# Optimization experiments

Measured on AMD Instinct MI355X. Metric: run time of the kernel, lower is better.

The kernel has to match this reference:

```python
import jax, jax.numpy as jnp
import numpy as np

B, T, D = 4, 50, 512
SRC, SENTS, WORDS = 400, 16, 40
NEG = jnp.float32(-1e30)  # stands in for -inf mask fill (numerically identical post-softmax)


def _seq_mask(lengths, max_len):
    # [n, max_len] bool, True where position < length
    return jnp.arange(max_len)[None, :] < lengths[:, None]


def _mlp_score(q, h, Wq, bq, Uc, v):
    # Bahdanau additive score: v^T tanh(W q + U h)
    # q: [b,t,d], h: [b,s,d] -> [b,t,s]
    wq = q @ Wq + bq                       # [b,t,d]
    uh = h @ Uc                            # [b,s,d]
    wquh = jnp.tanh(wq[:, :, None, :] + uh[:, None, :, :])  # [b,t,s,d]
    return jnp.einsum('btsd,d->bts', wquh, v)


def setup_inputs() -> dict:
    key = jax.random.key(0)
    ks = jax.random.split(key, 20)
    s = np.float32(1.0 / np.sqrt(D))
    def p(k, shape):
        return jax.random.normal(k, shape, jnp.float32) * s
    return {
        'source': jax.random.normal(ks[0], (B, T, D), jnp.float32),
        'src_bank': jax.random.normal(ks[1], (SRC, B, D), jnp.float32),
        'src_lengths': jax.random.randint(ks[2], (B,), 1, SRC + 1),
        'qa_sent_bank': jax.random.normal(ks[3], (SENTS, B, D), jnp.float32),
        'qa_sent_lengths': jax.random.randint(ks[4], (B,), 1, SENTS + 1),
        'qa_word_bank': jax.random.normal(ks[5], (WORDS, B, SENTS, D), jnp.float32),
        'qa_word_lengths': jax.random.randint(ks[6], (B, SENTS), 1, WORDS + 1),
        'Wq_word': p(ks[7], (D, D)), 'bq_word': jnp.zeros((D,), jnp.float32),
        'Uc_word': p(ks[8], (D, D)), 'v_word': p(ks[9], (D,)),
        'Wq_sent': p(ks[10], (D, D)), 'bq_sent': jnp.zeros((D,), jnp.float32),
        'Uc_sent': p(ks[11], (D, D)), 'v_sent': p(ks[12], (D,)),
        'Wq_pass': p(ks[13], (D, D)), 'bq_pass': jnp.zeros((D,), jnp.float32),
        'Uc_pass': p(ks[14], (D, D)), 'v_pass': p(ks[15], (D,)),
    }


def _forward(source, src_bank, qa_sent_bank, qa_word_bank,
             Wq_word, bq_word, Uc_word, v_word,
             Wq_sent, bq_sent, Uc_sent, v_sent,
             Wq_pass, bq_pass, Uc_pass, v_pass,
             src_lengths, qa_word_lengths):
    b = source.shape[0]
    # [words,b,sents,d] -> [b,sents,words,d] -> [b, sents*words, d]
    qa_word = jnp.transpose(qa_word_bank, (1, 2, 0, 3)).reshape(b, SENTS * WORDS, D)
    src = jnp.transpose(src_bank, (1, 0, 2))       # [b,src,d]
    sent = jnp.transpose(qa_sent_bank, (1, 0, 2))  # [b,sents,d]

    qa_word_align = _mlp_score(source, qa_word, Wq_word, bq_word, Uc_word, v_word)  # [b,t,sents*words]
    src_align = _mlp_score(source, src, Wq_pass, bq_pass, Uc_pass, v_pass)          # [b,t,src]
    qa_sent_align = _mlp_score(source, sent, Wq_sent, bq_sent, Uc_sent, v_sent)     # [b,t,sents]

    # hierarchical combination: word score scaled by its sentence score
    qa_hier = (qa_word_align.reshape(b, T, SENTS, WORDS)
               * qa_sent_align[..., None]).reshape(b, T, SENTS * WORDS)

    align = jnp.concatenate([src_align, qa_hier], axis=-1)  # [b,t,src+sents*words]

    qa_mask = _seq_mask(qa_word_lengths.reshape(-1), WORDS).reshape(b, SENTS * WORDS)[:, None, :]
    src_mask = _seq_mask(src_lengths, SRC)[:, None, :]
    mask = jnp.concatenate([src_mask, qa_mask], axis=-1)

    align = jnp.where(mask, align, NEG)
    align_vectors = jax.nn.softmax(align, axis=-1)  # joint length-masked softmax

    memory = jnp.concatenate([src, qa_word], axis=1)          # [b, src+sents*words, d]
    c = jnp.einsum('bts,bsd->btd', align_vectors, memory)     # weighted context sum
    return c


def reference(source, src_bank, src_lengths, qa_sent_bank, qa_sent_lengths,
              qa_word_bank, qa_word_lengths,
              Wq_word, bq_word, Uc_word, v_word,
              Wq_sent, bq_sent, Uc_sent, v_sent,
              Wq_pass, bq_pass, Uc_pass, v_pass):
    # qa_sent_lengths is accepted but unused, matching the original forward()
    return _forward(source, src_bank, qa_sent_bank, qa_word_bank,
                    Wq_word, bq_word, Uc_word, v_word,
                    Wq_sent, bq_sent, Uc_sent, v_sent,
                    Wq_pass, bq_pass, Uc_pass, v_pass,
                    src_lengths, qa_word_lengths)
```

## Files before the change

### kernel.cpp

```cpp
#include <hip/hip_runtime.h>
#include <hip/hip_bf16.h>


#define B_    4
#define T_    50
#define D_    512
#define SRC_  400
#define SENTS_ 16
#define WORDS_ 40
#define NW_   640
#define NMEM_ 1040
#define NK_   1056
#define NJOB_ 1056

#define C2L2E 2.8853900817779268f

typedef unsigned short ushort_t;
using s8v = __attribute__((ext_vector_type(8))) short;
using f4v = __attribute__((ext_vector_type(4))) float;

#define OFF_WQ_WORD 0
#define OFF_WQ_SENT 102400
#define OFF_WQ_PASS 204800
#define OFF_UH_SRC  307200
#define OFF_UH_WORD 1126400
#define OFF_UH_SENT 2437120
#define OFF_SC_SRC  2469888
#define OFF_SC_WORD 2549888
#define OFF_SC_SENT 2677888
#define P_BYTE_OFF  10724352ull
#define MT_BYTE_OFF 11265024ull
#define WT_BYTE_OFF 15590400ull

__device__ __forceinline__ ushort_t f2b(float f) {
    __hip_bfloat16 h = __float2bfloat16(f);
    return *(ushort_t*)&h;
}

__global__ __launch_bounds__(256) void k0f_transpose(
    const float* __restrict__ w0, const float* __restrict__ w1,
    const float* __restrict__ w2, const float* __restrict__ w3,
    const float* __restrict__ w4, const float* __restrict__ w5,
    const float* __restrict__ src_bank, const float* __restrict__ qa_word_bank,
    ushort_t* __restrict__ wt, ushort_t* __restrict__ mt)
{
    __shared__ float tile[32][33];
    int z = blockIdx.z;
    int tx = threadIdx.x & 31, ty = threadIdx.x >> 5;
    if (z < 6) {
        if (blockIdx.x >= 16) return;
        const float* W;
        switch (z) {
            case 0: W = w0; break; case 1: W = w1; break; case 2: W = w2; break;
            case 3: W = w3; break; case 4: W = w4; break; default: W = w5; break;
        }
        ushort_t* Wt = wt + z * (D_ * D_);
        int n0 = blockIdx.x * 32, k0 = blockIdx.y * 32;
#pragma unroll
        for (int a = 0; a < 4; ++a)
            tile[ty + a * 8][tx] = W[(k0 + ty + a * 8) * D_ + n0 + tx];
        __syncthreads();
#pragma unroll
        for (int a = 0; a < 4; ++a)
            Wt[(n0 + ty + a * 8) * D_ + k0 + tx] = f2b(tile[tx][ty + a * 8]);
    } else {
        int b = z - 6;
        int s0 = blockIdx.x * 32, d0 = blockIdx.y * 32;
#pragma unroll
        for (int a = 0; a < 4; ++a) {
            int s = s0 + ty + a * 8;
            float val = 0.f;
            if (s < SRC_) {
                val = src_bank[(s * B_ + b) * D_ + d0 + tx];
            } else if (s < NMEM_) {
                int j = s - SRC_; int se = j / WORDS_; int wd = j - se * WORDS_;
                val = qa_word_bank[((wd * B_ + b) * SENTS_ + se) * D_ + d0 + tx];
            }
            tile[ty + a * 8][tx] = val;
        }
        __syncthreads();
        ushort_t* base = mt + (size_t)b * D_ * NK_;
#pragma unroll
        for (int a = 0; a < 4; ++a) {
            int d = d0 + ty + a * 8;
            base[(size_t)d * NK_ + s0 + tx] = f2b(tile[tx][ty + a * 8]);
        }
    }
}

__global__ __launch_bounds__(256) void k1_gemm(
    const float* __restrict__ source, const float* __restrict__ src_bank,
    const float* __restrict__ qa_sent_bank, const float* __restrict__ qa_word_bank,
    const ushort_t* __restrict__ wt,
    const float* __restrict__ bq_word, const float* __restrict__ bq_sent,
    const float* __restrict__ bq_pass,
    float* __restrict__ wsf)
{
    __shared__ short At[64 * 32];
    __shared__ short Bt[64 * 32];
    int z = blockIdx.z;
    int M, atype; const float* bias; float* C;
    switch (z) {
        case 0: M = 200;  atype = 0; bias = bq_word; C = wsf + OFF_WQ_WORD; break;
        case 1: M = 200;  atype = 0; bias = bq_sent; C = wsf + OFF_WQ_SENT; break;
        case 2: M = 200;  atype = 0; bias = bq_pass; C = wsf + OFF_WQ_PASS; break;
        case 3: M = 2560; atype = 1; bias = nullptr; C = wsf + OFF_UH_WORD; break;
        case 4: M = 1600; atype = 2; bias = nullptr; C = wsf + OFF_UH_SRC;  break;
        default: M = 64;  atype = 3; bias = nullptr; C = wsf + OFF_UH_SENT; break;
    }
    int m0 = blockIdx.y * 64;
    if (m0 >= M) return;
    int n0 = blockIdx.x * 64;
    const ushort_t* W = wt + z * (D_ * D_);

    int tid = threadIdx.x;
    int lane = tid & 63, wv = tid >> 6;
    int quad = lane >> 4, l16 = lane & 15;
    int sm = tid >> 2, koff = (tid & 3) * 8;

    const float* arow = nullptr;
    {
        int r = m0 + sm;
        if (r < M) {
            if (atype == 0) arow = source + r * D_;
            else if (atype == 1) { int b = r / NW_; int j = r - b * NW_;
                                   int se = j / WORDS_; int wd = j - se * WORDS_;
                                   arow = qa_word_bank + ((wd * B_ + b) * SENTS_ + se) * D_; }
            else if (atype == 2) { int b = r / SRC_; int j = r - b * SRC_;
                                   arow = src_bank + (j * B_ + b) * D_; }
            else                 { int b = r >> 4; int s2 = r & 15;
                                   arow = qa_sent_bank + (s2 * B_ + b) * D_; }
        }
    }
    const ushort_t* wrow = W + (n0 + sm) * D_;

    f4v acc[4] = { {0.f,0.f,0.f,0.f}, {0.f,0.f,0.f,0.f},
                   {0.f,0.f,0.f,0.f}, {0.f,0.f,0.f,0.f} };

    for (int kk = 0; kk < 16; ++kk) {
        int k0 = kk * 32;
        union { ushort_t u[8]; int4 v; } pk;
        if (arow) {
            float4 f0 = *(const float4*)(arow + k0 + koff);
            float4 f1 = *(const float4*)(arow + k0 + koff + 4);
            pk.u[0] = f2b(f0.x); pk.u[1] = f2b(f0.y);
            pk.u[2] = f2b(f0.z); pk.u[3] = f2b(f0.w);
            pk.u[4] = f2b(f1.x); pk.u[5] = f2b(f1.y);
            pk.u[6] = f2b(f1.z); pk.u[7] = f2b(f1.w);
        } else {
            pk.v = int4{0, 0, 0, 0};
        }
        int4 bv = *(const int4*)(wrow + k0 + koff);
        *(int4*)(At + sm * 32 + koff) = pk.v;
        *(int4*)(Bt + sm * 32 + koff) = bv;
        __syncthreads();
        s8v af = *(const s8v*)(At + (wv * 16 + l16) * 32 + quad * 8);
#pragma unroll
        for (int ng = 0; ng < 4; ++ng) {
            s8v bf = *(const s8v*)(Bt + (ng * 16 + l16) * 32 + quad * 8);
            acc[ng] = __builtin_amdgcn_mfma_f32_16x16x32_bf16(af, bf, acc[ng], 0, 0, 0);
        }
        __syncthreads();
    }
#pragma unroll
    for (int ng = 0; ng < 4; ++ng) {
        int col = n0 + ng * 16 + l16;
        float bb = bias ? bias[col] : 0.f;
#pragma unroll
        for (int rr = 0; rr < 4; ++rr) {
            int row = m0 + wv * 16 + quad * 4 + rr;
            if (row < M) C[row * D_ + col] = (acc[ng][rr] + bb) * C2L2E;
        }
    }
}

__global__ __launch_bounds__(256) void k2_scores(
    const float* __restrict__ v_word, const float* __restrict__ v_sent,
    const float* __restrict__ v_pass,
    const int* __restrict__ src_lengths, const int* __restrict__ qa_word_lengths,
    float* __restrict__ wsf)
{
    int lane = threadIdx.x & 63;
    int job2 = blockIdx.x * 4 + (threadIdx.x >> 6);
    int job = job2 >> 1, th = job2 & 1;
    int b = job / NJOB_, slot = job - b * NJOB_;
    const float* uh; const float* v; const float* wq; float* out; int ostride;
    if (slot < SRC_) {
        if (slot >= src_lengths[b]) return;
        uh = wsf + OFF_UH_SRC + (b * SRC_ + slot) * D_;
        v = v_pass; wq = wsf + OFF_WQ_PASS + b * T_ * D_;
        out = wsf + OFF_SC_SRC + b * T_ * SRC_ + slot; ostride = SRC_;
    } else if (slot < NMEM_) {
        int j = slot - SRC_;
        int se = j / WORDS_; int wd = j - se * WORDS_;
        if (wd >= qa_word_lengths[b * SENTS_ + se]) return;
        uh = wsf + OFF_UH_WORD + (b * NW_ + j) * D_;
        v = v_word; wq = wsf + OFF_WQ_WORD + b * T_ * D_;
        out = wsf + OFF_SC_WORD + b * T_ * NW_ + j; ostride = NW_;
    } else {
        int s2 = slot - NMEM_;
        uh = wsf + OFF_UH_SENT + (b * SENTS_ + s2) * D_;
        v = v_sent; wq = wsf + OFF_WQ_SENT + b * T_ * D_;
        out = wsf + OFF_SC_SENT + b * T_ * SENTS_ + s2; ostride = SENTS_;
    }
    int d0 = lane * 8;
    float4 u0 = *(const float4*)(uh + d0);
    float4 u1 = *(const float4*)(uh + d0 + 4);
    float uhr[8] = {u0.x, u0.y, u0.z, u0.w, u1.x, u1.y, u1.z, u1.w};
    float4 v0 = *(const float4*)(v + d0);
    float4 v1 = *(const float4*)(v + d0 + 4);
    float vr[8] = {v0.x, v0.y, v0.z, v0.w, v1.x, v1.y, v1.z, v1.w};

    float vs = ((vr[0] + vr[1]) + (vr[2] + vr[3])) + ((vr[4] + vr[5]) + (vr[6] + vr[7]));
#pragma unroll
    for (int off = 32; off > 0; off >>= 1) vs += __shfl_xor(vs, off, 64);

    const float* wqh = wq + th * 25 * D_;
    float acc[25];
#pragma unroll 1
    for (int c = 0; c < 5; ++c) {
#pragma unroll
        for (int u5 = 0; u5 < 5; ++u5) {
            int u = c * 5 + u5;
            const float* wr = wqh + u * D_ + d0;
            float4 w0 = *(const float4*)(wr);
            float4 w1 = *(const float4*)(wr + 4);
            float wrr[8] = {w0.x, w0.y, w0.z, w0.w, w1.x, w1.y, w1.z, w1.w};
            float a = 0.f;
#pragma unroll
            for (int j = 0; j < 8; ++j) {
                float e = __builtin_amdgcn_exp2f(wrr[j] + uhr[j]);
                float r = __builtin_amdgcn_rcpf(e + 1.f);
                a = fmaf(vr[j], r, a);
            }
            acc[u] = a;
        }
    }
#pragma unroll
    for (int off = 32; off > 0; off >>= 1) {
#pragma unroll
        for (int u = 0; u < 25; ++u)
            acc[u] += __shfl_xor(acc[u], off, 64);
    }
    if (lane == 0) {
#pragma unroll
        for (int u = 0; u < 25; ++u)
            out[(th * 25 + u) * ostride] = fmaf(-2.f, acc[u], vs);
    }
}

__global__ __launch_bounds__(256) void k3a_softmax(
    const int* __restrict__ src_lengths, const int* __restrict__ qa_word_lengths,
    const float* __restrict__ wsf, ushort_t* __restrict__ P)
{
    __shared__ float p[NMEM_];
    __shared__ float red[4];
    int tid = threadIdx.x, lane = tid & 63, wv = tid >> 6;
    int bt = blockIdx.x, b = bt / T_, t = bt - b * T_;
    const float* sc_src  = wsf + OFF_SC_SRC  + bt * SRC_;
    const float* sc_word = wsf + OFF_SC_WORD + bt * NW_;
    const float* sc_sent = wsf + OFF_SC_SENT + bt * SENTS_;
    int slen = src_lengths[b];
    float mx = -3.0e38f;
    for (int j = tid; j < NMEM_; j += 256) {
        float val;
        if (j < SRC_) {
            val = (j < slen) ? sc_src[j] : -1e30f;
        } else {
            int jj = j - SRC_; int se = jj / WORDS_; int wd = jj - se * WORDS_;
            float raw = sc_word[jj] * sc_sent[se];
            val = (wd < qa_word_lengths[b * SENTS_ + se]) ? raw : -1e30f;
        }
        p[j] = val;
        mx = fmaxf(mx, val);
    }
#pragma unroll
    for (int off = 32; off > 0; off >>= 1) mx = fmaxf(mx, __shfl_xor(mx, off, 64));
    if (lane == 0) red[wv] = mx;
    __syncthreads();
    mx = fmaxf(fmaxf(red[0], red[1]), fmaxf(red[2], red[3]));
    __syncthreads();
    float lsum = 0.f;
    for (int j = tid; j < NMEM_; j += 256) {
        float e = __expf(p[j] - mx);
        p[j] = e; lsum += e;
    }
#pragma unroll
    for (int off = 32; off > 0; off >>= 1) lsum += __shfl_xor(lsum, off, 64);
    if (lane == 0) red[wv] = lsum;
    __syncthreads();
    float inv = 1.f / (red[0] + red[1] + red[2] + red[3]);
    ushort_t* prow = P + (size_t)(b * 64 + t) * NK_;
    for (int j = tid; j < NK_; j += 256)
        prow[j] = (j < NMEM_) ? f2b(p[j] * inv) : (ushort_t)0;
}

__global__ __launch_bounds__(256) void k3c_gemm(
    const ushort_t* __restrict__ P, const ushort_t* __restrict__ Mt,
    float* __restrict__ out)
{
    __shared__ short At[64 * 32];
    __shared__ short Bt[32 * 32];
    int b = blockIdx.y;
    int n0 = blockIdx.x * 32;
    int tid = threadIdx.x;
    int lane = tid & 63, wv = tid >> 6;
    int quad = lane >> 4, l16 = lane & 15;
    int smA = tid >> 2, koffA = (tid & 3) * 8;
    int smB = tid >> 3, koffB = (tid & 7) * 4;

    const ushort_t* arow = P + (size_t)(b * 64 + smA) * NK_ + koffA;
    const ushort_t* brow = Mt + ((size_t)(b * D_ + n0 + smB)) * NK_ + koffB;

    f4v acc[2] = { {0.f,0.f,0.f,0.f}, {0.f,0.f,0.f,0.f} };

    for (int kk = 0; kk < 33; ++kk) {
        int k0 = kk * 32;
        int4 av = *(const int4*)(arow + k0);
        int2 bv = *(const int2*)(brow + k0);
        *(int4*)(At + smA * 32 + koffA) = av;
        *(int2*)(Bt + smB * 32 + koffB) = bv;
        __syncthreads();
        s8v af = *(const s8v*)(At + (wv * 16 + l16) * 32 + quad * 8);
#pragma unroll
        for (int ng = 0; ng < 2; ++ng) {
            s8v bf = *(const s8v*)(Bt + (ng * 16 + l16) * 32 + quad * 8);
            acc[ng] = __builtin_amdgcn_mfma_f32_16x16x32_bf16(af, bf, acc[ng], 0, 0, 0);
        }
        __syncthreads();
    }
#pragma unroll
    for (int ng = 0; ng < 2; ++ng) {
        int col = n0 + ng * 16 + l16;
#pragma unroll
        for (int rr = 0; rr < 4; ++rr) {
            int row = wv * 16 + quad * 4 + rr;
            if (row < T_) out[(size_t)(b * T_ + row) * D_ + col] = acc[ng][rr];
        }
    }
}

extern "C" void kernel_launch(void* const* d_in, const int* in_sizes, int n_in,
                              void* d_out, int out_size, void* d_ws, size_t ws_size,
                              hipStream_t stream)
{
    (void)in_sizes; (void)n_in; (void)out_size; (void)ws_size;
    const float* source          = (const float*)d_in[0];
    const float* src_bank        = (const float*)d_in[1];
    const int*   src_lengths     = (const int*)d_in[2];
    const float* qa_sent_bank    = (const float*)d_in[3];
    const float* qa_word_bank    = (const float*)d_in[5];
    const int*   qa_word_lengths = (const int*)d_in[6];
    const float* Wq_word = (const float*)d_in[7];
    const float* bq_word = (const float*)d_in[8];
    const float* Uc_word = (const float*)d_in[9];
    const float* v_word  = (const float*)d_in[10];
    const float* Wq_sent = (const float*)d_in[11];
    const float* bq_sent = (const float*)d_in[12];
    const float* Uc_sent = (const float*)d_in[13];
    const float* v_sent  = (const float*)d_in[14];
    const float* Wq_pass = (const float*)d_in[15];
    const float* bq_pass = (const float*)d_in[16];
    const float* Uc_pass = (const float*)d_in[17];
    const float* v_pass  = (const float*)d_in[18];

    float* wsf = (float*)d_ws;
    ushort_t* Pb  = (ushort_t*)((char*)d_ws + P_BYTE_OFF);
    ushort_t* mt  = (ushort_t*)((char*)d_ws + MT_BYTE_OFF);
    ushort_t* wt  = (ushort_t*)((char*)d_ws + WT_BYTE_OFF);
    float* out = (float*)d_out;

    k0f_transpose<<<dim3(33, 16, 10), dim3(256), 0, stream>>>(
        Wq_word, Wq_sent, Wq_pass, Uc_word, Uc_pass, Uc_sent,
        src_bank, qa_word_bank, wt, mt);
    k1_gemm<<<dim3(8, 40, 6), dim3(256), 0, stream>>>(
        source, src_bank, qa_sent_bank, qa_word_bank, wt,
        bq_word, bq_sent, bq_pass, wsf);
    k2_scores<<<dim3(NJOB_ * 2), dim3(256), 0, stream>>>(
        v_word, v_sent, v_pass, src_lengths, qa_word_lengths, wsf);
    k3a_softmax<<<dim3(200), dim3(256), 0, stream>>>(src_lengths, qa_word_lengths, wsf, Pb);
    k3c_gemm<<<dim3(16, 4), dim3(256), 0, stream>>>(Pb, mt, out);
}
```

Baseline: 166.1 us.

## Fuse weight transpose into projection GEMM and softmax into context GEMM

The separate weight-transpose kernel is removed: the projection GEMM now reads fp32 weights directly, stages them through a swizzled shared tile, converts them to bf16 in the B-operand layout, and software-pipelines global loads one to two k-steps ahead. The memory-transpose blocks are folded into the same launch. The softmax kernel and its bf16 probability buffer are removed: the context GEMM computes per-row max and sum itself, then builds the exp-normalised probabilities on the fly while double-buffering score and memory loads. The score kernel now reduces in groups of five to cut register pressure. This saves two launches and the P and Wt round trips, but the 64 context blocks each recompute softmax statistics and do exp work inside the GEMM loop.

```diff
diff --git a/kernel.cpp b/kernel.cpp
--- a/kernel.cpp
+++ b/kernel.cpp
@@ -28,44 +28,33 @@
 #define OFF_SC_SRC  2469888
 #define OFF_SC_WORD 2549888
 #define OFF_SC_SENT 2677888
-#define P_BYTE_OFF  10724352ull
 #define MT_BYTE_OFF 11265024ull
-#define WT_BYTE_OFF 15590400ull
 
 __device__ __forceinline__ ushort_t f2b(float f) {
     __hip_bfloat16 h = __float2bfloat16(f);
     return *(ushort_t*)&h;
 }
 
-__global__ __launch_bounds__(256) void k0f_transpose(
+__global__ __launch_bounds__(256) void kA(
+    const float* __restrict__ source, const float* __restrict__ src_bank,
+    const float* __restrict__ qa_sent_bank, const float* __restrict__ qa_word_bank,
     const float* __restrict__ w0, const float* __restrict__ w1,
     const float* __restrict__ w2, const float* __restrict__ w3,
     const float* __restrict__ w4, const float* __restrict__ w5,
-    const float* __restrict__ src_bank, const float* __restrict__ qa_word_bank,
-    ushort_t* __restrict__ wt, ushort_t* __restrict__ mt)
+    const float* __restrict__ bq_word, const float* __restrict__ bq_sent,
+    const float* __restrict__ bq_pass,
+    float* __restrict__ wsf, ushort_t* __restrict__ mt)
 {
-    __shared__ float tile[32][33];
-    int z = blockIdx.z;
-    int tx = threadIdx.x & 31, ty = threadIdx.x >> 5;
-    if (z < 6) {
-        if (blockIdx.x >= 16) return;
-        const float* W;
-        switch (z) {
-            case 0: W = w0; break; case 1: W = w1; break; case 2: W = w2; break;
-            case 3: W = w3; break; case 4: W = w4; break; default: W = w5; break;
-        }
-        ushort_t* Wt = wt + z * (D_ * D_);
-        int n0 = blockIdx.x * 32, k0 = blockIdx.y * 32;
-#pragma unroll
-        for (int a = 0; a < 4; ++a)
-            tile[ty + a * 8][tx] = W[(k0 + ty + a * 8) * D_ + n0 + tx];
-        __syncthreads();
-#pragma unroll
-        for (int a = 0; a < 4; ++a)
-            Wt[(n0 + ty + a * 8) * D_ + k0 + tx] = f2b(tile[tx][ty + a * 8]);
-    } else {
-        int b = z - 6;
-        int s0 = blockIdx.x * 32, d0 = blockIdx.y * 32;
+    __shared__ float smemf[4224];
+    int bid = blockIdx.x;
+    int tid = threadIdx.x;
+
+    if (bid >= 1920) {
+        int tb = bid - 1920;
+        int b = tb / 528, r = tb - b * 528;
+        int s0 = (r % 33) * 32, d0 = (r / 33) * 32;
+        float (*tile)[33] = (float(*)[33])smemf;
+        int tx = tid & 31, ty = tid >> 5;
 #pragma unroll
         for (int a = 0; a < 4; ++a) {
             int s = s0 + ty + a * 8;
@@ -85,76 +74,113 @@
             int d = d0 + ty + a * 8;
             base[(size_t)d * NK_ + s0 + tx] = f2b(tile[tx][ty + a * 8]);
         }
-    }
-}
-
-__global__ __launch_bounds__(256) void k1_gemm(
-    const float* __restrict__ source, const float* __restrict__ src_bank,
-    const float* __restrict__ qa_sent_bank, const float* __restrict__ qa_word_bank,
-    const ushort_t* __restrict__ wt,
-    const float* __restrict__ bq_word, const float* __restrict__ bq_sent,
-    const float* __restrict__ bq_pass,
-    float* __restrict__ wsf)
-{
-    __shared__ short At[64 * 32];
-    __shared__ short Bt[64 * 32];
-    int z = blockIdx.z;
-    int M, atype; const float* bias; float* C;
+        return;
+    }
+
+    int z = bid / 320, rem = bid - z * 320;
+    int by = rem >> 3, bx = rem & 7;
+    int M, atype; const float* bias; const float* W; float* C;
     switch (z) {
-        case 0: M = 200;  atype = 0; bias = bq_word; C = wsf + OFF_WQ_WORD; break;
-        case 1: M = 200;  atype = 0; bias = bq_sent; C = wsf + OFF_WQ_SENT; break;
-        case 2: M = 200;  atype = 0; bias = bq_pass; C = wsf + OFF_WQ_PASS; break;
-        case 3: M = 2560; atype = 1; bias = nullptr; C = wsf + OFF_UH_WORD; break;
-        case 4: M = 1600; atype = 2; bias = nullptr; C = wsf + OFF_UH_SRC;  break;
-        default: M = 64;  atype = 3; bias = nullptr; C = wsf + OFF_UH_SENT; break;
-    }
-    int m0 = blockIdx.y * 64;
+        case 0: M = 200;  atype = 0; bias = bq_word; W = w0; C = wsf + OFF_WQ_WORD; break;
+        case 1: M = 200;  atype = 0; bias = bq_sent; W = w1; C = wsf + OFF_WQ_SENT; break;
+        case 2: M = 200;  atype = 0; bias = bq_pass; W = w2; C = wsf + OFF_WQ_PASS; break;
+        case 3: M = 2560; atype = 1; bias = nullptr; W = w3; C = wsf + OFF_UH_WORD; break;
+        case 4: M = 1600; atype = 2; bias = nullptr; W = w4; C = wsf + OFF_UH_SRC;  break;
+        default: M = 64;  atype = 3; bias = nullptr; W = w5; C = wsf + OFF_UH_SENT; break;
+    }
+    int m0 = by * 64;
     if (m0 >= M) return;
-    int n0 = blockIdx.x * 64;
-    const ushort_t* W = wt + z * (D_ * D_);
-
-    int tid = threadIdx.x;
-    int lane = tid & 63, wv = tid >> 6;
-    int quad = lane >> 4, l16 = lane & 15;
+    int n0 = bx * 64;
+
+    int lane = tid & 63, wvx = tid >> 6, quad = lane >> 4, l16 = lane & 15;
     int sm = tid >> 2, koff = (tid & 3) * 8;
+    int rW = tid >> 3, cW = (tid & 7) * 8;
+    int rWs = rW * 68 + (cW ^ (((rW >> 3) & 3) << 4));
+    int nB = tid >> 2, kB8 = (tid & 3) * 8;
+    int colp = nB ^ (((kB8 >> 3) & 3) << 4);
+
+    short* At = (short*)smemf;
+    short* Bt = (short*)(smemf + 1024);
+    float* Wtmp = smemf + 2048;
 
     const float* arow = nullptr;
     {
-        int r = m0 + sm;
-        if (r < M) {
-            if (atype == 0) arow = source + r * D_;
-            else if (atype == 1) { int b = r / NW_; int j = r - b * NW_;
+        int rr = m0 + sm;
+        if (rr < M) {
+            if (atype == 0) arow = source + rr * D_;
+            else if (atype == 1) { int b = rr / NW_; int j = rr - b * NW_;
                                    int se = j / WORDS_; int wd = j - se * WORDS_;
                                    arow = qa_word_bank + ((wd * B_ + b) * SENTS_ + se) * D_; }
-            else if (atype == 2) { int b = r / SRC_; int j = r - b * SRC_;
+            else if (atype == 2) { int b = rr / SRC_; int j = rr - b * SRC_;
                                    arow = src_bank + (j * B_ + b) * D_; }
-            else                 { int b = r >> 4; int s2 = r & 15;
+            else                 { int b = rr >> 4; int s2 = rr & 15;
                                    arow = qa_sent_bank + (s2 * B_ + b) * D_; }
         }
     }
-    const ushort_t* wrow = W + (n0 + sm) * D_;
+    const float* wbase = W + n0 + cW;
+
+    auto loadA = [&](float* r, int kk) {
+        if (arow) {
+            float4 f0 = *(const float4*)(arow + kk * 32 + koff);
+            float4 f1 = *(const float4*)(arow + kk * 32 + koff + 4);
+            r[0]=f0.x; r[1]=f0.y; r[2]=f0.z; r[3]=f0.w;
+            r[4]=f1.x; r[5]=f1.y; r[6]=f1.z; r[7]=f1.w;
+        } else {
+#pragma unroll
+            for (int i = 0; i < 8; ++i) r[i] = 0.f;
+        }
+    };
+    auto loadW = [&](float* r, int kk) {
+        const float* p = wbase + (kk * 32 + rW) * D_;
+        float4 f0 = *(const float4*)p;
+        float4 f1 = *(const float4*)(p + 4);
+        r[0]=f0.x; r[1]=f0.y; r[2]=f0.z; r[3]=f0.w;
+        r[4]=f1.x; r[5]=f1.y; r[6]=f1.z; r[7]=f1.w;
+    };
+    auto storeWtmp = [&](const float* r) {
+        *(float4*)(Wtmp + rWs)     = float4{r[0], r[1], r[2], r[3]};
+        *(float4*)(Wtmp + rWs + 4) = float4{r[4], r[5], r[6], r[7]};
+    };
+    auto storeAt = [&](const float* r) {
+        union { ushort_t u[8]; int4 v; } pk;
+#pragma unroll
+        for (int i = 0; i < 8; ++i) pk.u[i] = f2b(r[i]);
+        *(int4*)(At + sm * 32 + koff) = pk.v;
+    };
+    auto buildBt = [&]() {
+        union { ushort_t u[8]; int4 v; } pk;
+#pragma unroll
+        for (int i = 0; i < 8; ++i) pk.u[i] = f2b(Wtmp[(kB8 + i) * 68 + colp]);
+        *(int4*)(Bt + nB * 32 + kB8) = pk.v;
+    };
 
     f4v acc[4] = { {0.f,0.f,0.f,0.f}, {0.f,0.f,0.f,0.f},
                    {0.f,0.f,0.f,0.f}, {0.f,0.f,0.f,0.f} };
 
+    float ac[8], an[8], wn[8];
+    loadA(ac, 0);
+    {
+        float w0r[8];
+        loadW(w0r, 0);
+        storeWtmp(w0r);
+    }
+    loadW(wn, 1);
+    loadA(an, 1);
+    __syncthreads();
+
+#pragma unroll
     for (int kk = 0; kk < 16; ++kk) {
-        int k0 = kk * 32;
-        union { ushort_t u[8]; int4 v; } pk;
-        if (arow) {
-            float4 f0 = *(const float4*)(arow + k0 + koff);
-            float4 f1 = *(const float4*)(arow + k0 + koff + 4);
-            pk.u[0] = f2b(f0.x); pk.u[1] = f2b(f0.y);
-            pk.u[2] = f2b(f0.z); pk.u[3] = f2b(f0.w);
-            pk.u[4] = f2b(f1.x); pk.u[5] = f2b(f1.y);
-            pk.u[6] = f2b(f1.z); pk.u[7] = f2b(f1.w);
-        } else {
-            pk.v = int4{0, 0, 0, 0};
-        }
-        int4 bv = *(const int4*)(wrow + k0 + koff);
-        *(int4*)(At + sm * 32 + koff) = pk.v;
-        *(int4*)(Bt + sm * 32 + koff) = bv;
+        storeAt(ac);
+        buildBt();
         __syncthreads();
-        s8v af = *(const s8v*)(At + (wv * 16 + l16) * 32 + quad * 8);
+        if (kk < 15) storeWtmp(wn);
+        if (kk < 14) loadW(wn, kk + 2);
+        if (kk < 15) {
+#pragma unroll
+            for (int i = 0; i < 8; ++i) ac[i] = an[i];
+        }
+        if (kk < 14) loadA(an, kk + 2);
+        s8v af = *(const s8v*)(At + (wvx * 16 + l16) * 32 + quad * 8);
 #pragma unroll
         for (int ng = 0; ng < 4; ++ng) {
             s8v bf = *(const s8v*)(Bt + (ng * 16 + l16) * 32 + quad * 8);
@@ -162,19 +188,20 @@
         }
         __syncthreads();
     }
+
 #pragma unroll
     for (int ng = 0; ng < 4; ++ng) {
         int col = n0 + ng * 16 + l16;
         float bb = bias ? bias[col] : 0.f;
 #pragma unroll
-        for (int rr = 0; rr < 4; ++rr) {
-            int row = m0 + wv * 16 + quad * 4 + rr;
-            if (row < M) C[row * D_ + col] = (acc[ng][rr] + bb) * C2L2E;
+        for (int rr2 = 0; rr2 < 4; ++rr2) {
+            int row = m0 + wvx * 16 + quad * 4 + rr2;
+            if (row < M) C[row * D_ + col] = (acc[ng][rr2] + bb) * C2L2E;
         }
     }
 }
 
-__global__ __launch_bounds__(256) void k2_scores(
+__global__ __launch_bounds__(256) void kB_scores(
     const float* __restrict__ v_word, const float* __restrict__ v_sent,
     const float* __restrict__ v_pass,
     const int* __restrict__ src_lengths, const int* __restrict__ qa_word_lengths,
@@ -216,13 +243,12 @@
     for (int off = 32; off > 0; off >>= 1) vs += __shfl_xor(vs, off, 64);
 
     const float* wqh = wq + th * 25 * D_;
-    float acc[25];
 #pragma unroll 1
-    for (int c = 0; c < 5; ++c) {
+    for (int g = 0; g < 5; ++g) {
+        float a5[5];
 #pragma unroll
         for (int u5 = 0; u5 < 5; ++u5) {
-            int u = c * 5 + u5;
-            const float* wr = wqh + u * D_ + d0;
+            const float* wr = wqh + (g * 5 + u5) * D_ + d0;
             float4 w0 = *(const float4*)(wr);
             float4 w1 = *(const float4*)(wr + 4);
             float wrr[8] = {w0.x, w0.y, w0.z, w0.w, w1.x, w1.y, w1.z, w1.w};
@@ -233,109 +259,163 @@
                 float r = __builtin_amdgcn_rcpf(e + 1.f);
                 a = fmaf(vr[j], r, a);
             }
-            acc[u] = a;
-        }
-    }
-#pragma unroll
-    for (int off = 32; off > 0; off >>= 1) {
-#pragma unroll
-        for (int u = 0; u < 25; ++u)
-            acc[u] += __shfl_xor(acc[u], off, 64);
-    }
-    if (lane == 0) {
-#pragma unroll
-        for (int u = 0; u < 25; ++u)
-            out[(th * 25 + u) * ostride] = fmaf(-2.f, acc[u], vs);
+            a5[u5] = a;
+        }
+#pragma unroll
+        for (int off = 32; off > 0; off >>= 1) {
+#pragma unroll
+            for (int u5 = 0; u5 < 5; ++u5) a5[u5] += __shfl_xor(a5[u5], off, 64);
+        }
+        if (lane == 0) {
+#pragma unroll
+            for (int u5 = 0; u5 < 5; ++u5)
+                out[(th * 25 + g * 5 + u5) * ostride] = fmaf(-2.f, a5[u5], vs);
+        }
     }
 }
 
-__global__ __launch_bounds__(256) void k3a_softmax(
+__global__ __launch_bounds__(256) void kC_ctx(
     const int* __restrict__ src_lengths, const int* __restrict__ qa_word_lengths,
-    const float* __restrict__ wsf, ushort_t* __restrict__ P)
-{
-    __shared__ float p[NMEM_];
-    __shared__ float red[4];
-    int tid = threadIdx.x, lane = tid & 63, wv = tid >> 6;
-    int bt = blockIdx.x, b = bt / T_, t = bt - b * T_;
-    const float* sc_src  = wsf + OFF_SC_SRC  + bt * SRC_;
-    const float* sc_word = wsf + OFF_SC_WORD + bt * NW_;
-    const float* sc_sent = wsf + OFF_SC_SENT + bt * SENTS_;
-    int slen = src_lengths[b];
-    float mx = -3.0e38f;
-    for (int j = tid; j < NMEM_; j += 256) {
-        float val;
-        if (j < SRC_) {
-            val = (j < slen) ? sc_src[j] : -1e30f;
-        } else {
-            int jj = j - SRC_; int se = jj / WORDS_; int wd = jj - se * WORDS_;
-            float raw = sc_word[jj] * sc_sent[se];
-            val = (wd < qa_word_lengths[b * SENTS_ + se]) ? raw : -1e30f;
-        }
-        p[j] = val;
-        mx = fmaxf(mx, val);
-    }
-#pragma unroll
-    for (int off = 32; off > 0; off >>= 1) mx = fmaxf(mx, __shfl_xor(mx, off, 64));
-    if (lane == 0) red[wv] = mx;
-    __syncthreads();
-    mx = fmaxf(fmaxf(red[0], red[1]), fmaxf(red[2], red[3]));
-    __syncthreads();
-    float lsum = 0.f;
-    for (int j = tid; j < NMEM_; j += 256) {
-        float e = __expf(p[j] - mx);
-        p[j] = e; lsum += e;
-    }
-#pragma unroll
-    for (int off = 32; off > 0; off >>= 1) lsum += __shfl_xor(lsum, off, 64);
-    if (lane == 0) red[wv] = lsum;
-    __syncthreads();
-    float inv = 1.f / (red[0] + red[1] + red[2] + red[3]);
-    ushort_t* prow = P + (size_t)(b * 64 + t) * NK_;
-    for (int j = tid; j < NK_; j += 256)
-        prow[j] = (j < NMEM_) ? f2b(p[j] * inv) : (ushort_t)0;
-}
-
-__global__ __launch_bounds__(256) void k3c_gemm(
-    const ushort_t* __restrict__ P, const ushort_t* __restrict__ Mt,
+    const float* __restrict__ wsf, const ushort_t* __restrict__ Mt,
     float* __restrict__ out)
 {
     __shared__ short At[64 * 32];
     __shared__ short Bt[32 * 32];
-    int b = blockIdx.y;
-    int n0 = blockIdx.x * 32;
-    int tid = threadIdx.x;
-    int lane = tid & 63, wv = tid >> 6;
+    __shared__ float sentsL[T_ * SENTS_];
+    __shared__ float mxL[64];
+    __shared__ float invL[64];
+    __shared__ int lensL[SENTS_];
+    int tid = threadIdx.x, lane = tid & 63, wvx = tid >> 6;
     int quad = lane >> 4, l16 = lane & 15;
+    int b = blockIdx.y, n0 = blockIdx.x * 32;
+    int slen = src_lengths[b];
+
+    for (int i = tid; i < T_ * SENTS_; i += 256)
+        sentsL[i] = wsf[OFF_SC_SENT + b * (T_ * SENTS_) + i];
+    if (tid < SENTS_) lensL[tid] = qa_word_lengths[b * SENTS_ + tid];
+    if (tid >= 50 && tid < 64) { mxL[tid] = 0.f; invL[tid] = 0.f; }
+    __syncthreads();
+
+    const float* scs_b = wsf + OFF_SC_SRC + b * (T_ * SRC_);
+    const float* scw_b = wsf + OFF_SC_WORD + b * (T_ * NW_);
+
+    for (int t0 = wvx; t0 < T_; t0 += 8) {
+#pragma unroll
+        for (int tt = 0; tt < 2; ++tt) {
+            int t = t0 + tt * 4;
+            if (t < T_) {
+                const float* scs = scs_b + t * SRC_;
+                const float* scw = scw_b + t * NW_;
+                const float* srow = sentsL + t * SENTS_;
+                float vals[17];
+                float mxl = -3.0e38f;
+#pragma unroll
+                for (int i = 0; i < 17; ++i) {
+                    int j = lane + i * 64;
+                    float val = -1e30f;
+                    if (j < SRC_) {
+                        if (j < slen) val = scs[j];
+                    } else if (j < NMEM_) {
+                        int jj = j - SRC_; int se = jj / WORDS_; int wd = jj - se * WORDS_;
+                        if (wd < lensL[se]) val = scw[jj] * srow[se];
+                    }
+                    vals[i] = val;
+                    mxl = fmaxf(mxl, val);
+                }
+#pragma unroll
+                for (int off = 32; off > 0; off >>= 1)
+                    mxl = fmaxf(mxl, __shfl_xor(mxl, off, 64));
+                float s = 0.f;
+#pragma unroll
+                for (int i = 0; i < 17; ++i) s += __expf(vals[i] - mxl);
+#pragma unroll
+                for (int off = 32; off > 0; off >>= 1) s += __shfl_xor(s, off, 64);
+                if (lane == 0) { mxL[t] = mxl; invL[t] = 1.f / s; }
+            }
+        }
+    }
+    __syncthreads();
+
     int smA = tid >> 2, koffA = (tid & 3) * 8;
     int smB = tid >> 3, koffB = (tid & 7) * 4;
-
-    const ushort_t* arow = P + (size_t)(b * 64 + smA) * NK_ + koffA;
+    bool rowOK = smA < T_;
+    float mxT = mxL[smA], invT = invL[smA];
+    const float* scs = scs_b + (rowOK ? smA : 0) * SRC_;
+    const float* scw = scw_b + (rowOK ? smA : 0) * NW_;
+    const float* srowA = sentsL + (rowOK ? smA : 0) * SENTS_;
     const ushort_t* brow = Mt + ((size_t)(b * D_ + n0 + smB)) * NK_ + koffB;
 
-    f4v acc[2] = { {0.f,0.f,0.f,0.f}, {0.f,0.f,0.f,0.f} };
+    auto loadS = [&](float* r, int kk) {
+        int j0 = kk * 32 + koffA;
+        if (rowOK && j0 < NMEM_) {
+            const float* p = (j0 < SRC_) ? (scs + j0) : (scw + (j0 - SRC_));
+            float4 f0 = *(const float4*)p;
+            float4 f1 = *(const float4*)(p + 4);
+            r[0]=f0.x; r[1]=f0.y; r[2]=f0.z; r[3]=f0.w;
+            r[4]=f1.x; r[5]=f1.y; r[6]=f1.z; r[7]=f1.w;
+        } else {
+#pragma unroll
+            for (int i = 0; i < 8; ++i) r[i] = 0.f;
+        }
+    };
+    auto buildAt = [&](const float* r, int kk) {
+        int j0 = kk * 32 + koffA;
+        union { ushort_t u[8]; int4 v; } pk;
+        if (rowOK && j0 < NMEM_) {
+            if (j0 < SRC_) {
+#pragma unroll
+                for (int e = 0; e < 8; ++e) {
+                    float p = (j0 + e < slen) ? __expf(r[e] - mxT) * invT : 0.f;
+                    pk.u[e] = f2b(p);
+                }
+            } else {
+                int jj0 = j0 - SRC_;
+#pragma unroll
+                for (int e = 0; e < 8; ++e) {
+                    int jj = jj0 + e; int se = jj / WORDS_; int wd = jj - se * WORDS_;
+                    float p = (wd < lensL[se]) ? __expf(r[e] * srowA[se] - mxT) * invT : 0.f;
+                    pk.u[e] = f2b(p);
+                }
+            }
+        } else {
+            pk.v = int4{0, 0, 0, 0};
+        }
+        *(int4*)(At + smA * 32 + koffA) = pk.v;
+    };
+
+    f4v acc2[2] = { {0.f,0.f,0.f,0.f}, {0.f,0.f,0.f,0.f} };
+    float sc[8], sn[8];
+    int2 bc, bn;
+    loadS(sc, 0);
+    bc = *(const int2*)(brow);
 
     for (int kk = 0; kk < 33; ++kk) {
-        int k0 = kk * 32;
-        int4 av = *(const int4*)(arow + k0);
-        int2 bv = *(const int2*)(brow + k0);
-        *(int4*)(At + smA * 32 + koffA) = av;
-        *(int2*)(Bt + smB * 32 + koffB) = bv;
+        buildAt(sc, kk);
+        *(int2*)(Bt + smB * 32 + koffB) = bc;
         __syncthreads();
-        s8v af = *(const s8v*)(At + (wv * 16 + l16) * 32 + quad * 8);
+        if (kk < 32) {
+            loadS(sn, kk + 1);
+            bn = *(const int2*)(brow + (kk + 1) * 32);
+        }
+        s8v af = *(const s8v*)(At + (wvx * 16 + l16) * 32 + quad * 8);
 #pragma unroll
         for (int ng = 0; ng < 2; ++ng) {
             s8v bf = *(const s8v*)(Bt + (ng * 16 + l16) * 32 + quad * 8);
-            acc[ng] = __builtin_amdgcn_mfma_f32_16x16x32_bf16(af, bf, acc[ng], 0, 0, 0);
+            acc2[ng] = __builtin_amdgcn_mfma_f32_16x16x32_bf16(af, bf, acc2[ng], 0, 0, 0);
         }
         __syncthreads();
-    }
+#pragma unroll
+        for (int i = 0; i < 8; ++i) sc[i] = sn[i];
+        bc = bn;
+    }
+
 #pragma unroll
     for (int ng = 0; ng < 2; ++ng) {
         int col = n0 + ng * 16 + l16;
 #pragma unroll
-        for (int rr = 0; rr < 4; ++rr) {
-            int row = wv * 16 + quad * 4 + rr;
-            if (row < T_) out[(size_t)(b * T_ + row) * D_ + col] = acc[ng][rr];
+        for (int rr2 = 0; rr2 < 4; ++rr2) {
+            int row = wvx * 16 + quad * 4 + rr2;
+            if (row < T_) out[(size_t)(b * T_ + row) * D_ + col] = acc2[ng][rr2];
         }
     }
 }
@@ -365,19 +445,15 @@
     const float* v_pass  = (const float*)d_in[18];
 
     float* wsf = (float*)d_ws;
-    ushort_t* Pb  = (ushort_t*)((char*)d_ws + P_BYTE_OFF);
-    ushort_t* mt  = (ushort_t*)((char*)d_ws + MT_BYTE_OFF);
-    ushort_t* wt  = (ushort_t*)((char*)d_ws + WT_BYTE_OFF);
+    ushort_t* mt = (ushort_t*)((char*)d_ws + MT_BYTE_OFF);
     float* out = (float*)d_out;
 
-    k0f_transpose<<<dim3(33, 16, 10), dim3(256), 0, stream>>>(
+    kA<<<dim3(4032), dim3(256), 0, stream>>>(
+        source, src_bank, qa_sent_bank, qa_word_bank,
         Wq_word, Wq_sent, Wq_pass, Uc_word, Uc_pass, Uc_sent,
-        src_bank, qa_word_bank, wt, mt);
-    k1_gemm<<<dim3(8, 40, 6), dim3(256), 0, stream>>>(
-        source, src_bank, qa_sent_bank, qa_word_bank, wt,
-        bq_word, bq_sent, bq_pass, wsf);
-    k2_scores<<<dim3(NJOB_ * 2), dim3(256), 0, stream>>>(
+        bq_word, bq_sent, bq_pass, wsf, mt);
+    kB_scores<<<dim3(NJOB_ * 2), dim3(256), 0, stream>>>(
         v_word, v_sent, v_pass, src_lengths, qa_word_lengths, wsf);
-    k3a_softmax<<<dim3(200), dim3(256), 0, stream>>>(src_lengths, qa_word_lengths, wsf, Pb);
-    k3c_gemm<<<dim3(16, 4), dim3(256), 0, stream>>>(Pb, mt, out);
+    kC_ctx<<<dim3(16, 4), dim3(256), 0, stream>>>(
+        src_lengths, qa_word_lengths, wsf, mt, out);
 }
```

Result: slower. 218.1 us (+31.3%).

## Compact launch grids, prefetch GEMM tiles in registers, and chunk score reductions

Applied to the files above, without the earlier changes.

Replaces the 3D launch grids of the transpose and projection GEMM kernels with flat 1D grids that map block ids to work directly, so idle early-exit blocks are no longer launched. Adds register prefetching of global tiles two or three k-steps ahead in both bf16 MFMA GEMM loops, so global loads overlap the MFMA work instead of sitting just before the barrier. The score kernel now reduces and stores in groups of five rows rather than holding 25 accumulators, which lowers register pressure. The cost is more live registers for the prefetch buffers and extra index arithmetic.

```diff
diff --git a/kernel.cpp b/kernel.cpp
--- a/kernel.cpp
+++ b/kernel.cpp
@@ -45,17 +45,17 @@
     ushort_t* __restrict__ wt, ushort_t* __restrict__ mt)
 {
     __shared__ float tile[32][33];
-    int z = blockIdx.z;
+    int bid = blockIdx.x;
     int tx = threadIdx.x & 31, ty = threadIdx.x >> 5;
-    if (z < 6) {
-        if (blockIdx.x >= 16) return;
+    if (bid < 1536) {
+        int z = bid >> 8, r = bid & 255;
+        int n0 = (r & 15) * 32, k0 = (r >> 4) * 32;
         const float* W;
         switch (z) {
             case 0: W = w0; break; case 1: W = w1; break; case 2: W = w2; break;
             case 3: W = w3; break; case 4: W = w4; break; default: W = w5; break;
         }
         ushort_t* Wt = wt + z * (D_ * D_);
-        int n0 = blockIdx.x * 32, k0 = blockIdx.y * 32;
 #pragma unroll
         for (int a = 0; a < 4; ++a)
             tile[ty + a * 8][tx] = W[(k0 + ty + a * 8) * D_ + n0 + tx];
@@ -64,8 +64,9 @@
         for (int a = 0; a < 4; ++a)
             Wt[(n0 + ty + a * 8) * D_ + k0 + tx] = f2b(tile[tx][ty + a * 8]);
     } else {
-        int b = z - 6;
-        int s0 = blockIdx.x * 32, d0 = blockIdx.y * 32;
+        int tb = bid - 1536;
+        int b = tb / 528, r = tb - b * 528;
+        int s0 = (r % 33) * 32, d0 = (r / 33) * 32;
 #pragma unroll
         for (int a = 0; a < 4; ++a) {
             int s = s0 + ty + a * 8;
@@ -98,7 +99,13 @@
 {
     __shared__ short At[64 * 32];
     __shared__ short Bt[64 * 32];
-    int z = blockIdx.z;
+    int bid = blockIdx.x;
+    int z, rem;
+    if (bid < 96)       { z = bid >> 5; rem = bid & 31; }
+    else if (bid < 416) { z = 3; rem = bid - 96; }
+    else if (bid < 616) { z = 4; rem = bid - 416; }
+    else                { z = 5; rem = bid - 616; }
+    int by = rem >> 3, bx = rem & 7;
     int M, atype; const float* bias; float* C;
     switch (z) {
         case 0: M = 200;  atype = 0; bias = bq_word; C = wsf + OFF_WQ_WORD; break;
@@ -108,9 +115,7 @@
         case 4: M = 1600; atype = 2; bias = nullptr; C = wsf + OFF_UH_SRC;  break;
         default: M = 64;  atype = 3; bias = nullptr; C = wsf + OFF_UH_SENT; break;
     }
-    int m0 = blockIdx.y * 64;
-    if (m0 >= M) return;
-    int n0 = blockIdx.x * 64;
+    int m0 = by * 64, n0 = bx * 64;
     const ushort_t* W = wt + z * (D_ * D_);
 
     int tid = threadIdx.x;
@@ -134,26 +139,40 @@
     }
     const ushort_t* wrow = W + (n0 + sm) * D_;
 
+    auto loadA = [&](float* r, int kk) {
+        if (arow) {
+            float4 f0 = *(const float4*)(arow + kk * 32 + koff);
+            float4 f1 = *(const float4*)(arow + kk * 32 + koff + 4);
+            r[0]=f0.x; r[1]=f0.y; r[2]=f0.z; r[3]=f0.w;
+            r[4]=f1.x; r[5]=f1.y; r[6]=f1.z; r[7]=f1.w;
+        } else {
+#pragma unroll
+            for (int i = 0; i < 8; ++i) r[i] = 0.f;
+        }
+    };
+
     f4v acc[4] = { {0.f,0.f,0.f,0.f}, {0.f,0.f,0.f,0.f},
                    {0.f,0.f,0.f,0.f}, {0.f,0.f,0.f,0.f} };
 
+    float a0[8], a1[8];
+    int4 w0v, w1v;
+    loadA(a0, 0); w0v = *(const int4*)(wrow + 0 * 32 + koff);
+    loadA(a1, 1); w1v = *(const int4*)(wrow + 1 * 32 + koff);
+
     for (int kk = 0; kk < 16; ++kk) {
-        int k0 = kk * 32;
         union { ushort_t u[8]; int4 v; } pk;
-        if (arow) {
-            float4 f0 = *(const float4*)(arow + k0 + koff);
-            float4 f1 = *(const float4*)(arow + k0 + koff + 4);
-            pk.u[0] = f2b(f0.x); pk.u[1] = f2b(f0.y);
-            pk.u[2] = f2b(f0.z); pk.u[3] = f2b(f0.w);
-            pk.u[4] = f2b(f1.x); pk.u[5] = f2b(f1.y);
-            pk.u[6] = f2b(f1.z); pk.u[7] = f2b(f1.w);
-        } else {
-            pk.v = int4{0, 0, 0, 0};
-        }
-        int4 bv = *(const int4*)(wrow + k0 + koff);
+#pragma unroll
+        for (int i = 0; i < 8; ++i) pk.u[i] = f2b(a0[i]);
         *(int4*)(At + sm * 32 + koff) = pk.v;
-        *(int4*)(Bt + sm * 32 + koff) = bv;
-        __syncthreads();
+        *(int4*)(Bt + sm * 32 + koff) = w0v;
+        __syncthreads();
+#pragma unroll
+        for (int i = 0; i < 8; ++i) a0[i] = a1[i];
+        w0v = w1v;
+        if (kk < 14) {
+            loadA(a1, kk + 2);
+            w1v = *(const int4*)(wrow + (kk + 2) * 32 + koff);
+        }
         s8v af = *(const s8v*)(At + (wv * 16 + l16) * 32 + quad * 8);
 #pragma unroll
         for (int ng = 0; ng < 4; ++ng) {
@@ -216,13 +235,12 @@
     for (int off = 32; off > 0; off >>= 1) vs += __shfl_xor(vs, off, 64);
 
     const float* wqh = wq + th * 25 * D_;
-    float acc[25];
 #pragma unroll 1
-    for (int c = 0; c < 5; ++c) {
+    for (int g = 0; g < 5; ++g) {
+        float a5[5];
 #pragma unroll
         for (int u5 = 0; u5 < 5; ++u5) {
-            int u = c * 5 + u5;
-            const float* wr = wqh + u * D_ + d0;
+            const float* wr = wqh + (g * 5 + u5) * D_ + d0;
             float4 w0 = *(const float4*)(wr);
             float4 w1 = *(const float4*)(wr + 4);
             float wrr[8] = {w0.x, w0.y, w0.z, w0.w, w1.x, w1.y, w1.z, w1.w};
@@ -233,19 +251,18 @@
                 float r = __builtin_amdgcn_rcpf(e + 1.f);
                 a = fmaf(vr[j], r, a);
             }
-            acc[u] = a;
-        }
-    }
-#pragma unroll
-    for (int off = 32; off > 0; off >>= 1) {
-#pragma unroll
-        for (int u = 0; u < 25; ++u)
-            acc[u] += __shfl_xor(acc[u], off, 64);
-    }
-    if (lane == 0) {
-#pragma unroll
-        for (int u = 0; u < 25; ++u)
-            out[(th * 25 + u) * ostride] = fmaf(-2.f, acc[u], vs);
+            a5[u5] = a;
+        }
+#pragma unroll
+        for (int off = 32; off > 0; off >>= 1) {
+#pragma unroll
+            for (int u5 = 0; u5 < 5; ++u5) a5[u5] += __shfl_xor(a5[u5], off, 64);
+        }
+        if (lane == 0) {
+#pragma unroll
+            for (int u5 = 0; u5 < 5; ++u5)
+                out[(th * 25 + g * 5 + u5) * ostride] = fmaf(-2.f, a5[u5], vs);
+        }
     }
 }
 
@@ -314,13 +331,22 @@
 
     f4v acc[2] = { {0.f,0.f,0.f,0.f}, {0.f,0.f,0.f,0.f} };
 
+    int4 a0 = *(const int4*)(arow);
+    int2 b0 = *(const int2*)(brow);
+    int4 a1 = *(const int4*)(arow + 32);
+    int2 b1 = *(const int2*)(brow + 32);
+    int4 a2 = *(const int4*)(arow + 64);
+    int2 b2 = *(const int2*)(brow + 64);
+
     for (int kk = 0; kk < 33; ++kk) {
-        int k0 = kk * 32;
-        int4 av = *(const int4*)(arow + k0);
-        int2 bv = *(const int2*)(brow + k0);
-        *(int4*)(At + smA * 32 + koffA) = av;
-        *(int2*)(Bt + smB * 32 + koffB) = bv;
-        __syncthreads();
+        *(int4*)(At + smA * 32 + koffA) = a0;
+        *(int2*)(Bt + smB * 32 + koffB) = b0;
+        __syncthreads();
+        a0 = a1; a1 = a2; b0 = b1; b1 = b2;
+        if (kk < 30) {
+            a2 = *(const int4*)(arow + (kk + 3) * 32);
+            b2 = *(const int2*)(brow + (kk + 3) * 32);
+        }
         s8v af = *(const s8v*)(At + (wv * 16 + l16) * 32 + quad * 8);
 #pragma unroll
         for (int ng = 0; ng < 2; ++ng) {
@@ -370,10 +396,10 @@
     ushort_t* wt  = (ushort_t*)((char*)d_ws + WT_BYTE_OFF);
     float* out = (float*)d_out;
 
-    k0f_transpose<<<dim3(33, 16, 10), dim3(256), 0, stream>>>(
+    k0f_transpose<<<dim3(3648), dim3(256), 0, stream>>>(
         Wq_word, Wq_sent, Wq_pass, Uc_word, Uc_pass, Uc_sent,
         src_bank, qa_word_bank, wt, mt);
-    k1_gemm<<<dim3(8, 40, 6), dim3(256), 0, stream>>>(
+    k1_gemm<<<dim3(624), dim3(256), 0, stream>>>(
         source, src_bank, qa_sent_bank, qa_word_bank, wt,
         bq_word, bq_sent, bq_pass, wsf);
     k2_scores<<<dim3(NJOB_ * 2), dim3(256), 0, stream>>>(
```

After: 154.7 us. -6.8%, faster.
